# Kernel optimization log

Hardware: AMD Instinct MI355X
Metric: run time of the kernel (lower is better)

The kernel has to match this reference:

```python
import jax, jax.numpy as jnp
import numpy as np

MAX_VISIT = 200
NUM_CODE = 506          # feature vocab -> 507 multi-hot dims
NUM_TGT = 284           # target vocab multi-hot dims
B = 64
P = 40                  # codes per visit
D_OTH = 57              # others feature dim (sign slice [37:] is 20-dim)
K = 100                 # len(weight_idx)
LSTM = 256
D_FEAT = (NUM_CODE + 1) + K + 27 + (D_OTH - 37)   # 654
D_FWD = D_FEAT + 10                                # 664
D_MLP_IN = (NUM_CODE + 1) + (D_OTH - 37) + 20 + 8  # 555


def multi_hot(codes, n):
    """Binary multi-hot encode int codes over last axis. codes: [..., P]."""
    shp = codes.shape
    flat = codes.reshape(-1, shp[-1])
    R = flat.shape[0]
    rows = jnp.repeat(jnp.arange(R), shp[-1])
    z = jnp.zeros((R, n), jnp.float32).at[rows, flat.reshape(-1)].set(1.0)
    return z.reshape(shp[:-1] + (n,))


def reverse_sequence(x, lengths):
    """tf.reverse_sequence along axis 1: reverse first lengths[i] steps, keep rest."""
    T = x.shape[1]
    j = jnp.arange(T)[None, :]
    L = lengths[:, None]
    idx = jnp.where(j < L, L - 1 - j, j)          # [B, T]
    return jnp.take_along_axis(x, idx[:, :, None], axis=1)


def setup_inputs() -> dict:
    key = jax.random.key(0)
    ks = jax.random.split(key, 13)
    code = jax.random.randint(ks[0], (B, MAX_VISIT, P), 0, NUM_CODE + 1, dtype=jnp.int32)
    others = jax.random.normal(ks[1], (B, MAX_VISIT, D_OTH), jnp.float32)
    length = jax.random.randint(ks[2], (B,), 3, MAX_VISIT + 1, dtype=jnp.int32)
    target = jax.random.randint(ks[3], (B, 10), 0, NUM_TGT, dtype=jnp.int32)
    weight_idx = jax.random.randint(ks[4], (K,), 0, NUM_TGT, dtype=jnp.int32)
    s = 0.02
    Wf = jax.random.normal(ks[5], (D_FWD, LSTM), jnp.float32) * s
    bf = jnp.zeros((LSTM,), jnp.float32)
    Wb = jax.random.normal(ks[6], (D_FWD, LSTM), jnp.float32) * s
    bb = jnp.zeros((LSTM,), jnp.float32)
    W0 = jax.random.normal(ks[7], (D_MLP_IN, 256), jnp.float32) * s
    b0 = jnp.zeros((256,), jnp.float32)
    W1 = jax.random.normal(ks[8], (256, 256), jnp.float32) * s
    b1 = jnp.zeros((256,), jnp.float32)
    return {"code": code, "others": others, "length": length, "target": target,
            "weight_idx": weight_idx, "Wf": Wf, "bf": bf, "Wb": Wb, "bb": bb,
            "W0": W0, "b0": b0, "W1": W1, "b1": b1}


def reference(code, others, length, target, weight_idx, Wf, bf, Wb, bb, W0, b0, W1, b1):
    code_mh = multi_hot(code, NUM_CODE + 1)                      # [B,200,507]
    # valid-visit mask (dense analogue of tf.boolean_mask over [B,198])
    mask = (jnp.arange(MAX_VISIT - 2)[None, :] < (length - 2)[:, None]).astype(jnp.float32)
    sign = others[:, 1:-1, 37:]                                  # [B,198,20]
    interval_ = jnp.concatenate([others[:, 1:-1, 27:37], others[:, 2:, 27:37]], axis=-1)
    stay = others[:, 1:-1, 19:27]
    x = jnp.concatenate([code_mh[:, 1:-1], sign, interval_, stay], axis=-1)  # [B,198,555]
    h = jax.nn.relu(x @ W0 + b0) @ W1 + b1                       # [B,198,256]
    fv = h / jnp.sqrt(jnp.sum(h * h, axis=-1, keepdims=True))
    fv = fv * mask[:, :, None]                                   # zero invalid rows
    # target block: gather (1 - multi-hot) at weight_idx, tile over visits
    tgt = 1.0 - multi_hot(target, NUM_TGT)                       # [B,284]
    tgt = tgt[:, weight_idx]                                     # [B,K]
    tgt = jnp.broadcast_to(tgt[:, None, :], (B, MAX_VISIT, K))
    code_full = jnp.concatenate([code_mh, tgt], axis=-1)         # [B,200,607]
    interval = others[:, :, 27:37]
    interval_backward = jnp.concatenate(
        [jnp.zeros((B, 1, 10), jnp.float32), reverse_sequence(interval, length)[:, :-1]], axis=1)
    feature = jnp.concatenate([code_full, others[:, :, :27], others[:, :, 37:]], axis=-1)
    feature_backward = reverse_sequence(feature, length)
    x_forward = jnp.concatenate([feature, interval], axis=-1)[:, :-2] @ Wf + bf
    x_backward = jnp.concatenate([feature_backward, interval_backward], axis=-1)[:, :-2] @ Wb + bb
    return (x_forward, x_backward, fv)
```

## Files before the change

### kernel.cpp

```cpp
#include <hip/hip_runtime.h>
#include <hip/hip_bf16.h>

typedef unsigned short u16;
typedef __attribute__((ext_vector_type(8))) short short8;
typedef __attribute__((ext_vector_type(4))) float f32x4;

#define TMAX 200
#define TOUT 198
#define PC 40
#define DOTH 57
#define NKT 9
#define FWD_OFF 0
#define BWD_OFF 3244032
#define FV_OFF  6488064
#define OWF 0
#define OWB 294912
#define OW0 589824
#define OW1 884736
#define OTF 1015808
#define OTB 1081344

__device__ __forceinline__ u16 f2b(float v) {
  __hip_bfloat16 h = __float2bfloat16(v);
  return *(u16*)&h;
}

__global__ __launch_bounds__(256) void prep_kernel(
    const int* __restrict__ target, const int* __restrict__ widx,
    const float* __restrict__ Wf, const float* __restrict__ bfv,
    const float* __restrict__ Wb, const float* __restrict__ bbv,
    const float* __restrict__ W0, const float* __restrict__ W1,
    u16* __restrict__ wsu, float* __restrict__ wsf)
{
  int blk = blockIdx.x, n = threadIdx.x;
  if (blk < 248) {
    const float* src; u16* dst; int kb; int mode;
    if (blk < 72)       { src=Wf; dst=wsu+OWF/2; kb=blk;     mode=0; }
    else if (blk < 144) { src=Wb; dst=wsu+OWB/2; kb=blk-72;  mode=0; }
    else if (blk < 216) { src=W0; dst=wsu+OW0/2; kb=blk-144; mode=1; }
    else                { src=W1; dst=wsu+OW1/2; kb=blk-216; mode=2; }
    u16 pk[8];
    #pragma unroll
    for (int j=0;j<8;j++) {
      int k = kb*8+j;
      int sr;
      if (mode==0)      sr = (k<57)? 607+k : (k<564)? k-57 : -1;
      else if (mode==1) sr = (k<48)? 507+k : (k<57)? -1 : (k<564)? k-57 : -1;
      else              sr = k;
      float v = (sr>=0)? src[sr*256+n] : 0.f;
      pk[j] = f2b(v);
    }
    *(uint4*)(dst + (kb*256+n)*8) = *(uint4*)pk;
  } else {
    int b = blk - 248;
    __shared__ float tval[100]; __shared__ int tg[10];
    if (n<10) tg[n]=target[b*10+n];
    __syncthreads();
    if (n<100){ int w=widx[n]; float v=1.f;
      #pragma unroll
      for(int i=0;i<10;i++) if(tg[i]==w) v=0.f;
      tval[n]=v; }
    __syncthreads();
    float aF=bfv[n], aB=bbv[n];
    for(int k=0;k<100;k++){ float v=tval[k];
      aF=fmaf(v,Wf[(507+k)*256+n],aF); aB=fmaf(v,Wb[(507+k)*256+n],aB); }
    wsf[OTF/4 + b*256+n]=aF; wsf[OTB/4 + b*256+n]=aB;
  }
}

__global__ __launch_bounds__(256, 4) void gemm_kernel(
    const int* __restrict__ code, const float* __restrict__ others,
    const int* __restrict__ length,
    const float* __restrict__ b0, const float* __restrict__ b1,
    const u16* __restrict__ wsu, const float* __restrict__ wsf,
    float* __restrict__ out)
{
  const int tile = blockIdx.x;
  const int strm = blockIdx.y;
  const int tid = threadIdx.x;
  const int wv = tid>>6, lane = tid&63, q = lane>>4, c = lane&15;
  const int colbase = wv*64 + c;

  __shared__ u16 lA[3][2048];
  __shared__ int rowB[32], rowT[32], rowS[32], rowS2[32], rowL[32];
  __shared__ float rpart[4][32];

  if (tid < 32) {
    int m = tile*32 + tid;
    int b = m/198, t = m - b*198;
    int L = length[b];
    int s, s2 = 0;
    if (strm==0) s = t;
    else if (strm==1){ s = (t<L)? (L-1-t) : t;
                       s2 = (t==0)? -1 : (((t-1)<L)? (L-t) : (t-1)); }
    else s = t+1;
    rowB[tid]=b; rowT[tid]=t; rowS[tid]=s; rowS2[tid]=s2; rowL[tid]=L;
  }
  __syncthreads();

  int mys[5];
  #pragma unroll
  for (int it=0; it<5; it++) {
    int idx = tid + it*256;
    int r = idx/40, p = idx - r*40;
    mys[it] = (57 + code[(rowB[r]*TMAX + rowS[r])*PC + p]) | (r<<19);
  }

  float dv[8];
  if (strm < 2) {
    #pragma unroll
    for (int it=0; it<8; it++) {
      int idx = tid + it*256;
      float v = 0.f;
      if (idx < 32*57) {
        int r = idx/57, j = idx - r*57;
        int col = (j<27)? j : (j<47)? 37+(j-27) : 27+(j-47);
        int sr = (strm==1 && j>=47)? rowS2[r] : rowS[r];
        if (sr >= 0) v = others[(rowB[r]*TMAX + sr)*DOTH + col];
      }
      dv[it] = v;
    }
  } else {
    #pragma unroll
    for (int it=0; it<6; it++) {
      int idx = tid + it*256;
      int r = idx/48, j = idx - r*48;
      int t = rowT[r], srow, col;
      if (j<20)      { srow=t+1; col=37+j; }
      else if (j<30) { srow=t+1; col=27+(j-20); }
      else if (j<40) { srow=t+2; col=27+(j-30); }
      else           { srow=t+1; col=19+(j-40); }
      dv[it] = others[(rowB[r]*TMAX + srow)*DOTH + col];
    }
  }

  { uint4 z = {0,0,0,0};
    ((uint4*)lA[0])[tid] = z; ((uint4*)lA[1])[tid] = z; }
  __syncthreads();
  #pragma unroll
  for (int it=0; it<5; it++) {
    unsigned d = (unsigned)(mys[it] & 0xFFFF);
    if (d < 64u) lA[0][(d>>3)*256 + (mys[it]>>16) + (d&7)] = 0x3F80;
  }
  if (strm < 2) {
    #pragma unroll
    for (int it=0; it<8; it++) {
      int idx = tid + it*256;
      if (idx < 32*57) {
        int r = idx/57, j = idx - r*57;
        lA[0][(j>>3)*256 + r*8 + (j&7)] = f2b(dv[it]);
      }
    }
  } else {
    #pragma unroll
    for (int it=0; it<6; it++) {
      int idx = tid + it*256;
      int r = idx/48, j = idx - r*48;
      lA[0][(j>>3)*256 + r*8 + (j&7)] = f2b(dv[it]);
    }
  }

  f32x4 acc[2][4];
  if (strm < 2) {
    const float* tg = wsf + ((strm==0)? OTF/4 : OTB/4);
    #pragma unroll
    for (int mt=0; mt<2; mt++)
      #pragma unroll
      for (int reg=0; reg<4; reg++) {
        int rl = mt*16 + q*4 + reg;
        const float* tr = tg + rowB[rl]*256;
        #pragma unroll
        for (int nt=0; nt<4; nt++) acc[mt][nt][reg] = tr[colbase + nt*16];
      }
  } else {
    #pragma unroll
    for (int nt=0; nt<4; nt++){ float v = b0[colbase + nt*16];
      #pragma unroll
      for (int mt=0; mt<2; mt++)
        #pragma unroll
        for (int reg=0; reg<4; reg++) acc[mt][nt][reg]=v; }
  }
  __syncthreads();

  const u16* Wpk = wsu + ((strm==0)? OWF/2 : (strm==1)? OWB/2 : OW0/2);
  for (int kt=0; kt<NKT; kt++) {
    const u16* A = lA[kt%3];
    const u16* gB0 = Wpk + ((kt*8 + q    )*256 + colbase)*8;
    const u16* gB1 = Wpk + ((kt*8 + 4 + q)*256 + colbase)*8;
    short8 bf0[4], bf1[4];
    #pragma unroll
    for (int nt=0; nt<4; nt++) bf0[nt] = *(const short8*)(gB0 + nt*16*8);
    #pragma unroll
    for (int nt=0; nt<4; nt++) bf1[nt] = *(const short8*)(gB1 + nt*16*8);
    if (kt < 8) {
      u16* nb = lA[(kt+1)%3];
      const int k0n = (kt+1)*64;
      #pragma unroll
      for (int it=0; it<5; it++) {
        unsigned d = (unsigned)((mys[it] & 0xFFFF) - k0n);
        if (d < 64u) nb[(d>>3)*256 + (mys[it]>>16) + (d&7)] = 0x3F80;
      }
    }
    if (kt < 7) {
      uint4 z = {0,0,0,0};
      ((uint4*)lA[(kt+2)%3])[tid] = z;
    }
    short8 af0[2], af1[2];
    #pragma unroll
    for (int mt=0; mt<2; mt++) af0[mt] = *(const short8*)&A[(q    )*256 + (mt*16 + c)*8];
    #pragma unroll
    for (int mt=0; mt<2; mt++) af1[mt] = *(const short8*)&A[(4 + q)*256 + (mt*16 + c)*8];
    #pragma unroll
    for (int mt=0; mt<2; mt++)
      #pragma unroll
      for (int nt=0; nt<4; nt++)
        acc[mt][nt] = __builtin_amdgcn_mfma_f32_16x16x32_bf16(af0[mt], bf0[nt], acc[mt][nt], 0,0,0);
    #pragma unroll
    for (int mt=0; mt<2; mt++)
      #pragma unroll
      for (int nt=0; nt<4; nt++)
        acc[mt][nt] = __builtin_amdgcn_mfma_f32_16x16x32_bf16(af1[mt], bf1[nt], acc[mt][nt], 0,0,0);
    __syncthreads();
  }

  if (strm < 2) {
    float* o = out + ((strm==0)? FWD_OFF : BWD_OFF);
    #pragma unroll
    for (int mt=0; mt<2; mt++)
      #pragma unroll
      for (int reg=0; reg<4; reg++) {
        int rl = mt*16 + q*4 + reg;
        float* orow = o + (rowB[rl]*TOUT + rowT[rl])*256 + colbase;
        #pragma unroll
        for (int nt=0; nt<4; nt++) orow[nt*16] = acc[mt][nt][reg];
      }
  } else {
    if (wv == 0) {
      #pragma unroll
      for (int mt=0; mt<2; mt++)
        #pragma unroll
        for (int reg=0; reg<4; reg++) {
          int rl = mt*16 + q*4 + reg;
          #pragma unroll
          for (int nt=0; nt<4; nt++) {
            int kl = c + nt*16;
            lA[0][(kl>>3)*256 + rl*8 + (kl&7)] = f2b(fmaxf(acc[mt][nt][reg], 0.f));
          }
        }
    }
    __syncthreads();
    f32x4 a2[2][4];
    #pragma unroll
    for (int nt=0; nt<4; nt++){ float v = b1[colbase + nt*16];
      #pragma unroll
      for (int mt=0; mt<2; mt++)
        #pragma unroll
        for (int reg=0; reg<4; reg++) a2[mt][nt][reg]=v; }
    const u16* W1p = wsu + OW1/2;
    for (int kt2=0; kt2<4; kt2++) {
      if (wv == kt2+1) {
        u16* B2 = lA[(kt2+1)&1];
        #pragma unroll
        for (int mt=0; mt<2; mt++)
          #pragma unroll
          for (int reg=0; reg<4; reg++) {
            int rl = mt*16 + q*4 + reg;
            #pragma unroll
            for (int nt=0; nt<4; nt++) {
              int kl = c + nt*16;
              B2[(kl>>3)*256 + rl*8 + (kl&7)] = f2b(fmaxf(acc[mt][nt][reg], 0.f));
            }
          }
      }
      const u16* A2 = lA[kt2&1];
      #pragma unroll
      for (int s=0; s<2; s++) {
        int akb = s*4 + q;
        const u16* gB = W1p + ((kt2*8 + akb)*256 + colbase)*8;
        short8 af[2], bf[4];
        #pragma unroll
        for (int nt=0; nt<4; nt++) bf[nt] = *(const short8*)(gB + nt*16*8);
        #pragma unroll
        for (int mt=0; mt<2; mt++) af[mt] = *(const short8*)&A2[akb*256 + (mt*16 + c)*8];
        #pragma unroll
        for (int mt=0; mt<2; mt++)
          #pragma unroll
          for (int nt=0; nt<4; nt++)
            a2[mt][nt] = __builtin_amdgcn_mfma_f32_16x16x32_bf16(af[mt], bf[nt], a2[mt][nt], 0,0,0);
      }
      __syncthreads();
    }
    #pragma unroll
    for (int mt=0; mt<2; mt++)
      #pragma unroll
      for (int reg=0; reg<4; reg++) {
        int rl = mt*16 + q*4 + reg;
        float ss = 0.f;
        #pragma unroll
        for (int nt=0; nt<4; nt++){ float v=a2[mt][nt][reg]; ss = fmaf(v,v,ss); }
        ss += __shfl_xor(ss, 1, 64); ss += __shfl_xor(ss, 2, 64);
        ss += __shfl_xor(ss, 4, 64); ss += __shfl_xor(ss, 8, 64);
        if (c==0) rpart[wv][rl] = ss;
      }
    __syncthreads();
    #pragma unroll
    for (int mt=0; mt<2; mt++)
      #pragma unroll
      for (int reg=0; reg<4; reg++) {
        int rl = mt*16 + q*4 + reg;
        float s = rpart[0][rl]+rpart[1][rl]+rpart[2][rl]+rpart[3][rl];
        float inv = (s>0.f)? (1.0f/sqrtf(s)) : 0.f;
        int t = rowT[rl];
        if (t >= rowL[rl]-2) inv = 0.f;
        float* orow = out + FV_OFF + (rowB[rl]*TOUT + t)*256 + colbase;
        #pragma unroll
        for (int nt=0; nt<4; nt++) orow[nt*16] = a2[mt][nt][reg]*inv;
      }
  }
}

extern "C" void kernel_launch(void* const* d_in, const int* in_sizes, int n_in,
                              void* d_out, int out_size, void* d_ws, size_t ws_size,
                              hipStream_t stream) {
  const int*   code    = (const int*)d_in[0];
  const float* others  = (const float*)d_in[1];
  const int*   length  = (const int*)d_in[2];
  const int*   target  = (const int*)d_in[3];
  const int*   widx    = (const int*)d_in[4];
  const float* Wf      = (const float*)d_in[5];
  const float* bfv     = (const float*)d_in[6];
  const float* Wb      = (const float*)d_in[7];
  const float* bbv     = (const float*)d_in[8];
  const float* W0      = (const float*)d_in[9];
  const float* b0v     = (const float*)d_in[10];
  const float* W1      = (const float*)d_in[11];
  const float* b1v     = (const float*)d_in[12];

  u16*   wsu = (u16*)d_ws;
  float* wsf = (float*)d_ws;
  float* out = (float*)d_out;

  prep_kernel<<<dim3(312), dim3(256), 0, stream>>>(target, widx, Wf, bfv, Wb, bbv, W0, W1, wsu, wsf);
  gemm_kernel<<<dim3(396,3), dim3(256), 0, stream>>>(code, others, length,
      b0v, b1v, wsu, wsf, out);
}
```

Baseline: 123.7 us.

## Replace per-k-tile LDS multi-hot staging with register-expanded bitmasks

The multi-hot code block is now stored as a per-row bitmask in shared memory, built with atomicOr, and expanded directly into bf16 MFMA A-fragments in registers. This removes the triple-buffered LDS A tiles and the __syncthreads in every k-iteration of the main GEMM loop, which is now fully unrolled. The row metadata tables are replaced by recomputing b, t and length per use, and the bias and target addends are applied in the epilogue instead of initialising the accumulators. In exchange it adds LDS atomics, bit-expansion ALU work and extra integer divides and global reads of length.

```diff
diff --git a/kernel.cpp b/kernel.cpp
--- a/kernel.cpp
+++ b/kernel.cpp
@@ -2,6 +2,7 @@
 #include <hip/hip_bf16.h>
 
 typedef unsigned short u16;
+typedef unsigned long long u64;
 typedef __attribute__((ext_vector_type(8))) short short8;
 typedef __attribute__((ext_vector_type(4))) float f32x4;
 
@@ -9,7 +10,6 @@
 #define TOUT 198
 #define PC 40
 #define DOTH 57
-#define NKT 9
 #define FWD_OFF 0
 #define BWD_OFF 3244032
 #define FV_OFF  6488064
@@ -23,6 +23,13 @@
 __device__ __forceinline__ u16 f2b(float v) {
   __hip_bfloat16 h = __float2bfloat16(v);
   return *(u16*)&h;
+}
+
+__device__ __forceinline__ short8 expand8(unsigned byte) {
+  short8 v;
+  #pragma unroll
+  for (int j = 0; j < 8; j++) v[j] = ((byte >> j) & 1u) ? (short)0x3F80 : (short)0;
+  return v;
 }
 
 __global__ __launch_bounds__(256) void prep_kernel(
@@ -81,29 +88,24 @@
   const int wv = tid>>6, lane = tid&63, q = lane>>4, c = lane&15;
   const int colbase = wv*64 + c;
 
-  __shared__ u16 lA[3][2048];
-  __shared__ int rowB[32], rowT[32], rowS[32], rowS2[32], rowL[32];
+  __shared__ u16 lA[2048];
+  __shared__ u16 lH[2][2048];
+  __shared__ unsigned bm[32][18];
   __shared__ float rpart[4][32];
-
-  if (tid < 32) {
-    int m = tile*32 + tid;
-    int b = m/198, t = m - b*198;
-    int L = length[b];
-    int s, s2 = 0;
-    if (strm==0) s = t;
-    else if (strm==1){ s = (t<L)? (L-1-t) : t;
-                       s2 = (t==0)? -1 : (((t-1)<L)? (L-t) : (t-1)); }
-    else s = t+1;
-    rowB[tid]=b; rowT[tid]=t; rowS[tid]=s; rowS2[tid]=s2; rowL[tid]=L;
-  }
-  __syncthreads();
 
   int mys[5];
   #pragma unroll
   for (int it=0; it<5; it++) {
     int idx = tid + it*256;
     int r = idx/40, p = idx - r*40;
-    mys[it] = (57 + code[(rowB[r]*TMAX + rowS[r])*PC + p]) | (r<<19);
+    int m = tile*32 + r;
+    int b = m/198, t = m - b*198;
+    int L = length[b];
+    int s;
+    if (strm==0) s = t;
+    else if (strm==1) s = (t<L)? (L-1-t) : t;
+    else s = t+1;
+    mys[it] = (57 + code[(b*TMAX + s)*PC + p]) | (r<<16);
   }
 
   float dv[8];
@@ -114,9 +116,15 @@
       float v = 0.f;
       if (idx < 32*57) {
         int r = idx/57, j = idx - r*57;
+        int m = tile*32 + r;
+        int b = m/198, t = m - b*198;
+        int L = length[b];
         int col = (j<27)? j : (j<47)? 37+(j-27) : 27+(j-47);
-        int sr = (strm==1 && j>=47)? rowS2[r] : rowS[r];
-        if (sr >= 0) v = others[(rowB[r]*TMAX + sr)*DOTH + col];
+        int sr;
+        if (strm==0) sr = t;
+        else if (j < 47) sr = (t<L)? (L-1-t) : t;
+        else sr = (t==0)? -1 : (((t-1)<L)? (L-t) : (t-1));
+        if (sr >= 0) v = others[(b*TMAX + sr)*DOTH + col];
       }
       dv[it] = v;
     }
@@ -125,22 +133,30 @@
     for (int it=0; it<6; it++) {
       int idx = tid + it*256;
       int r = idx/48, j = idx - r*48;
-      int t = rowT[r], srow, col;
+      int m = tile*32 + r;
+      int b = m/198, t = m - b*198;
+      int srow, col;
       if (j<20)      { srow=t+1; col=37+j; }
       else if (j<30) { srow=t+1; col=27+(j-20); }
       else if (j<40) { srow=t+2; col=27+(j-30); }
       else           { srow=t+1; col=19+(j-40); }
-      dv[it] = others[(rowB[r]*TMAX + srow)*DOTH + col];
-    }
-  }
-
-  { uint4 z = {0,0,0,0};
-    ((uint4*)lA[0])[tid] = z; ((uint4*)lA[1])[tid] = z; }
+      dv[it] = others[(b*TMAX + srow)*DOTH + col];
+    }
+  }
+
+  { uint4 z = {0,0,0,0}; ((uint4*)lA)[tid] = z; }
+  for (int idx = tid; idx < 32*18; idx += 256) ((unsigned*)bm)[idx] = 0u;
   __syncthreads();
+
   #pragma unroll
   for (int it=0; it<5; it++) {
     unsigned d = (unsigned)(mys[it] & 0xFFFF);
-    if (d < 64u) lA[0][(d>>3)*256 + (mys[it]>>16) + (d&7)] = 0x3F80;
+    int r = mys[it] >> 16;
+    if (d < 64u) lA[(d>>3)*256 + r*8 + (d&7)] = 0x3F80;
+    else {
+      unsigned kb = d - 64u;
+      atomicOr(&bm[r][kb>>5], 1u << (kb & 31u));
+    }
   }
   if (strm < 2) {
     #pragma unroll
@@ -148,7 +164,7 @@
       int idx = tid + it*256;
       if (idx < 32*57) {
         int r = idx/57, j = idx - r*57;
-        lA[0][(j>>3)*256 + r*8 + (j&7)] = f2b(dv[it]);
+        lA[(j>>3)*256 + r*8 + (j&7)] = f2b(dv[it]);
       }
     }
   } else {
@@ -156,35 +172,46 @@
     for (int it=0; it<6; it++) {
       int idx = tid + it*256;
       int r = idx/48, j = idx - r*48;
-      lA[0][(j>>3)*256 + r*8 + (j&7)] = f2b(dv[it]);
-    }
-  }
+      lA[(j>>3)*256 + r*8 + (j&7)] = f2b(dv[it]);
+    }
+  }
+  __syncthreads();
 
   f32x4 acc[2][4];
-  if (strm < 2) {
-    const float* tg = wsf + ((strm==0)? OTF/4 : OTB/4);
-    #pragma unroll
-    for (int mt=0; mt<2; mt++)
-      #pragma unroll
-      for (int reg=0; reg<4; reg++) {
-        int rl = mt*16 + q*4 + reg;
-        const float* tr = tg + rowB[rl]*256;
-        #pragma unroll
-        for (int nt=0; nt<4; nt++) acc[mt][nt][reg] = tr[colbase + nt*16];
-      }
-  } else {
-    #pragma unroll
-    for (int nt=0; nt<4; nt++){ float v = b0[colbase + nt*16];
-      #pragma unroll
-      for (int mt=0; mt<2; mt++)
-        #pragma unroll
-        for (int reg=0; reg<4; reg++) acc[mt][nt][reg]=v; }
-  }
-  __syncthreads();
+  #pragma unroll
+  for (int mt=0; mt<2; mt++)
+    #pragma unroll
+    for (int nt=0; nt<4; nt++)
+      #pragma unroll
+      for (int reg=0; reg<4; reg++) acc[mt][nt][reg] = 0.f;
 
   const u16* Wpk = wsu + ((strm==0)? OWF/2 : (strm==1)? OWB/2 : OW0/2);
-  for (int kt=0; kt<NKT; kt++) {
-    const u16* A = lA[kt%3];
+  {
+    const u16* gB0 = Wpk + ((q    )*256 + colbase)*8;
+    const u16* gB1 = Wpk + ((4 + q)*256 + colbase)*8;
+    short8 bf0[4], bf1[4];
+    #pragma unroll
+    for (int nt=0; nt<4; nt++) bf0[nt] = *(const short8*)(gB0 + nt*16*8);
+    #pragma unroll
+    for (int nt=0; nt<4; nt++) bf1[nt] = *(const short8*)(gB1 + nt*16*8);
+    short8 af0[2], af1[2];
+    #pragma unroll
+    for (int mt=0; mt<2; mt++) af0[mt] = *(const short8*)&lA[(q    )*256 + (mt*16 + c)*8];
+    #pragma unroll
+    for (int mt=0; mt<2; mt++) af1[mt] = *(const short8*)&lA[(4 + q)*256 + (mt*16 + c)*8];
+    #pragma unroll
+    for (int mt=0; mt<2; mt++)
+      #pragma unroll
+      for (int nt=0; nt<4; nt++)
+        acc[mt][nt] = __builtin_amdgcn_mfma_f32_16x16x32_bf16(af0[mt], bf0[nt], acc[mt][nt], 0,0,0);
+    #pragma unroll
+    for (int mt=0; mt<2; mt++)
+      #pragma unroll
+      for (int nt=0; nt<4; nt++)
+        acc[mt][nt] = __builtin_amdgcn_mfma_f32_16x16x32_bf16(af1[mt], bf1[nt], acc[mt][nt], 0,0,0);
+  }
+  #pragma unroll
+  for (int kt=1; kt<9; kt++) {
     const u16* gB0 = Wpk + ((kt*8 + q    )*256 + colbase)*8;
     const u16* gB1 = Wpk + ((kt*8 + 4 + q)*256 + colbase)*8;
     short8 bf0[4], bf1[4];
@@ -192,47 +219,40 @@
     for (int nt=0; nt<4; nt++) bf0[nt] = *(const short8*)(gB0 + nt*16*8);
     #pragma unroll
     for (int nt=0; nt<4; nt++) bf1[nt] = *(const short8*)(gB1 + nt*16*8);
-    if (kt < 8) {
-      u16* nb = lA[(kt+1)%3];
-      const int k0n = (kt+1)*64;
-      #pragma unroll
-      for (int it=0; it<5; it++) {
-        unsigned d = (unsigned)((mys[it] & 0xFFFF) - k0n);
-        if (d < 64u) nb[(d>>3)*256 + (mys[it]>>16) + (d&7)] = 0x3F80;
-      }
-    }
-    if (kt < 7) {
-      uint4 z = {0,0,0,0};
-      ((uint4*)lA[(kt+2)%3])[tid] = z;
-    }
-    short8 af0[2], af1[2];
-    #pragma unroll
-    for (int mt=0; mt<2; mt++) af0[mt] = *(const short8*)&A[(q    )*256 + (mt*16 + c)*8];
-    #pragma unroll
-    for (int mt=0; mt<2; mt++) af1[mt] = *(const short8*)&A[(4 + q)*256 + (mt*16 + c)*8];
-    #pragma unroll
-    for (int mt=0; mt<2; mt++)
-      #pragma unroll
-      for (int nt=0; nt<4; nt++)
-        acc[mt][nt] = __builtin_amdgcn_mfma_f32_16x16x32_bf16(af0[mt], bf0[nt], acc[mt][nt], 0,0,0);
-    #pragma unroll
-    for (int mt=0; mt<2; mt++)
-      #pragma unroll
-      for (int nt=0; nt<4; nt++)
-        acc[mt][nt] = __builtin_amdgcn_mfma_f32_16x16x32_bf16(af1[mt], bf1[nt], acc[mt][nt], 0,0,0);
-    __syncthreads();
+    u64 w0 = *(const u64*)&bm[c][2*(kt-1)];
+    u64 w1 = *(const u64*)&bm[16+c][2*(kt-1)];
+    unsigned b00 = (unsigned)(w0 >> (q*8))        & 0xFFu;
+    unsigned b01 = (unsigned)(w0 >> (32 + q*8))   & 0xFFu;
+    unsigned b10 = (unsigned)(w1 >> (q*8))        & 0xFFu;
+    unsigned b11 = (unsigned)(w1 >> (32 + q*8))   & 0xFFu;
+    short8 a00 = expand8(b00), a01 = expand8(b01);
+    short8 a10 = expand8(b10), a11 = expand8(b11);
+    #pragma unroll
+    for (int nt=0; nt<4; nt++) {
+      acc[0][nt] = __builtin_amdgcn_mfma_f32_16x16x32_bf16(a00, bf0[nt], acc[0][nt], 0,0,0);
+      acc[1][nt] = __builtin_amdgcn_mfma_f32_16x16x32_bf16(a10, bf0[nt], acc[1][nt], 0,0,0);
+    }
+    #pragma unroll
+    for (int nt=0; nt<4; nt++) {
+      acc[0][nt] = __builtin_amdgcn_mfma_f32_16x16x32_bf16(a01, bf1[nt], acc[0][nt], 0,0,0);
+      acc[1][nt] = __builtin_amdgcn_mfma_f32_16x16x32_bf16(a11, bf1[nt], acc[1][nt], 0,0,0);
+    }
   }
 
   if (strm < 2) {
+    const float* tg = wsf + ((strm==0)? OTF/4 : OTB/4);
     float* o = out + ((strm==0)? FWD_OFF : BWD_OFF);
     #pragma unroll
     for (int mt=0; mt<2; mt++)
       #pragma unroll
       for (int reg=0; reg<4; reg++) {
         int rl = mt*16 + q*4 + reg;
-        float* orow = o + (rowB[rl]*TOUT + rowT[rl])*256 + colbase;
-        #pragma unroll
-        for (int nt=0; nt<4; nt++) orow[nt*16] = acc[mt][nt][reg];
+        int m = tile*32 + rl;
+        int b = m/198, t = m - b*198;
+        const float* tr = tg + b*256;
+        float* orow = o + (b*TOUT + t)*256 + colbase;
+        #pragma unroll
+        for (int nt=0; nt<4; nt++) orow[nt*16] = acc[mt][nt][reg] + tr[colbase + nt*16];
       }
   } else {
     if (wv == 0) {
@@ -244,7 +264,8 @@
           #pragma unroll
           for (int nt=0; nt<4; nt++) {
             int kl = c + nt*16;
-            lA[0][(kl>>3)*256 + rl*8 + (kl&7)] = f2b(fmaxf(acc[mt][nt][reg], 0.f));
+            lH[0][(kl>>3)*256 + rl*8 + (kl&7)] =
+                f2b(fmaxf(acc[mt][nt][reg] + b0[colbase + nt*16], 0.f));
           }
         }
     }
@@ -259,7 +280,7 @@
     const u16* W1p = wsu + OW1/2;
     for (int kt2=0; kt2<4; kt2++) {
       if (wv == kt2+1) {
-        u16* B2 = lA[(kt2+1)&1];
+        u16* B2 = lH[(kt2+1)&1];
         #pragma unroll
         for (int mt=0; mt<2; mt++)
           #pragma unroll
@@ -268,11 +289,12 @@
             #pragma unroll
             for (int nt=0; nt<4; nt++) {
               int kl = c + nt*16;
-              B2[(kl>>3)*256 + rl*8 + (kl&7)] = f2b(fmaxf(acc[mt][nt][reg], 0.f));
+              B2[(kl>>3)*256 + rl*8 + (kl&7)] =
+                  f2b(fmaxf(acc[mt][nt][reg] + b0[colbase + nt*16], 0.f));
             }
           }
       }
-      const u16* A2 = lA[kt2&1];
+      const u16* A2 = lH[kt2&1];
       #pragma unroll
       for (int s=0; s<2; s++) {
         int akb = s*4 + q;
@@ -310,9 +332,10 @@
         int rl = mt*16 + q*4 + reg;
         float s = rpart[0][rl]+rpart[1][rl]+rpart[2][rl]+rpart[3][rl];
         float inv = (s>0.f)? (1.0f/sqrtf(s)) : 0.f;
-        int t = rowT[rl];
-        if (t >= rowL[rl]-2) inv = 0.f;
-        float* orow = out + FV_OFF + (rowB[rl]*TOUT + t)*256 + colbase;
+        int m = tile*32 + rl;
+        int b = m/198, t = m - b*198;
+        if (t >= length[b]-2) inv = 0.f;
+        float* orow = out + FV_OFF + (b*TOUT + t)*256 + colbase;
         #pragma unroll
         for (int nt=0; nt<4; nt++) orow[nt*16] = a2[mt][nt][reg]*inv;
       }
```

Result: slower. 129.0 us (+4.3%).
